# Kernel tuning notes

Measured on AMD Instinct MI355X. Metric: run time of the kernel, lower is better.

Reference implementation:

```python
import jax, jax.numpy as jnp
import numpy as np


def gcn_conv(x, W, b, src, dst, w, num_nodes):
    """PyG GCNConv: out = D^{-1/2} (A + I) D^{-1/2} (x @ W) + b, edge weights w."""
    xw = x @ W  # [BN, out_dim]
    # degree with self-loop weight 1.0, accumulated at target nodes
    deg = jax.ops.segment_sum(w, dst, num_segments=num_nodes) + 1.0  # [BN]
    dinv = jax.lax.rsqrt(deg)
    norm = dinv[src] * w * dinv[dst]  # [E]
    agg = jax.ops.segment_sum(xw[src] * norm[:, None], dst, num_segments=num_nodes)
    agg = agg + xw * (dinv * dinv)[:, None]  # self-loop contribution
    return agg + b


def setup_inputs() -> dict:
    key = jax.random.key(0)
    ks = jax.random.split(key, 10)
    BN, E, D = 100000, 1600000, 128
    return {
        "x": jax.random.normal(ks[0], (BN, D), dtype=jnp.float32),
        "edge_index": jax.random.randint(ks[1], (2, E), 0, BN, dtype=jnp.int64),
        "B": 8,
        "N": 12500,
        "causal_edge_index": jax.random.randint(ks[2], (2, 16), 0, BN, dtype=jnp.int64),
        "edge_weight": jax.random.uniform(ks[3], (E,), dtype=jnp.float32),
        "causal_edge_weight": jax.random.uniform(ks[4], (16,), dtype=jnp.float32),
        "W1": jax.random.normal(ks[5], (D, D), dtype=jnp.float32) * (1.0 / np.sqrt(D)),
        "b1": jnp.zeros((D,), dtype=jnp.float32),
        "W2": jax.random.normal(ks[6], (D, D), dtype=jnp.float32) * (1.0 / np.sqrt(D)),
        "b2": jnp.zeros((D,), dtype=jnp.float32),
        "Wres": jax.random.normal(ks[7], (D, D), dtype=jnp.float32) * (1.0 / np.sqrt(D)),
        "bres": jnp.zeros((D,), dtype=jnp.float32),
    }


def reference(x, edge_index, B, N, causal_edge_index, edge_weight,
              causal_edge_weight, W1, b1, W2, b2, Wres, bres):
    BN = B * N
    src, dst = edge_index[0], edge_index[1]
    # layer 1: GCNConv -> gelu (dropout is identity in eval)
    h = gcn_conv(x, W1, b1, src, dst, edge_weight, BN)  # [BN, hidden]
    h = jax.nn.gelu(h, approximate=False)
    # residual: 0.3 * Linear(x)
    h = h + 0.3 * (x @ Wres + bres)
    # layer 2: GCNConv -> gelu
    out = gcn_conv(h, W2, b2, src, dst, edge_weight, BN)
    return jax.nn.gelu(out, approximate=False)
```

## Files before the change

### kernel.cpp

```cpp
#include <hip/hip_runtime.h>
#include <math.h>

#define DIM 128
#define SCAN_CHUNK 4096
#define NB_HALF 256

typedef __attribute__((ext_vector_type(8))) short short8;
typedef __attribute__((ext_vector_type(4))) float f32x4;

__device__ __forceinline__ float gelu_exact(float v) {
    return 0.5f * v * (1.0f + erff(v * 0.70710678118654752f));
}

__device__ __forceinline__ unsigned short f2bf(float f) {
    unsigned int u = __float_as_uint(f);
    return (unsigned short)((u + 0x7FFFu + ((u >> 16) & 1u)) >> 16);
}
__device__ __forceinline__ float bf_lo(unsigned int v) { return __uint_as_float(v << 16); }
__device__ __forceinline__ float bf_hi(unsigned int v) { return __uint_as_float(v & 0xFFFF0000u); }


__global__ void deg_cnt_kernel(const int* __restrict__ dst,
                               const float* __restrict__ w,
                               unsigned long long* __restrict__ packed,
                               int* __restrict__ rank, int E) {
    int e = blockIdx.x * blockDim.x + threadIdx.x;
    if (e >= E) return;
    int d = dst[e];
    unsigned long long inc =
        (1ull << 32) | (unsigned long long)(unsigned int)(w[e] * 67108864.0f);
    unsigned long long old = atomicAdd(&packed[d], inc);
    rank[e] = (int)(old >> 32);
}


__global__ __launch_bounds__(256) void wt3_kernel(const float* __restrict__ W1,
                                                  const float* __restrict__ Wres,
                                                  const float* __restrict__ W2,
                                                  unsigned short* __restrict__ Wt1,
                                                  unsigned short* __restrict__ Wtr,
                                                  unsigned short* __restrict__ Wt2) {
    int b = blockIdx.x;
    const float* W = (b < 64) ? W1 : (b < 128) ? Wres : W2;
    unsigned short* Wt = (b < 64) ? Wt1 : (b < 128) ? Wtr : Wt2;
    int idx = (b & 63) * 256 + threadIdx.x;
    int r = idx >> 7, c = idx & 127;
    Wt[c * 128 + r] = f2bf(W[idx]);
}


template <int MODE>
__device__ __forceinline__ void gemm_breg_body(const float* __restrict__ X,
                                               const unsigned short* __restrict__ Wt,
                                               const float* __restrict__ bias,
                                               unsigned short* __restrict__ outb,
                                               float* __restrict__ Bf,
                                               int BN, int t0, int tStride) {
    int tid = threadIdx.x;
    int wv = tid >> 6, l = tid & 63;
    int l15 = l & 15, kg = l >> 4;

    uint4 b[4][8];
#pragma unroll
    for (int ks = 0; ks < 4; ks++)
#pragma unroll
        for (int nt = 0; nt < 8; nt++)
            b[ks][nt] = *(const uint4*)(Wt + (size_t)(nt * 16 + l15) * 128 + ks * 32 + kg * 8);

    float bias_r[8];
    if (MODE == 2) {
#pragma unroll
        for (int nt = 0; nt < 8; nt++) bias_r[nt] = bias[nt * 16 + l15];
    }

    int nTiles = (BN + 63) / 64;

    float4 aRaw[8];
    {
        int rowA = t0 * 64 + wv * 16 + l15;
        if (rowA > BN - 1) rowA = BN - 1;
        const float* ap = X + (size_t)rowA * 128 + kg * 8;
#pragma unroll
        for (int ks = 0; ks < 4; ks++) {
            aRaw[2 * ks] = *(const float4*)(ap + ks * 32);
            aRaw[2 * ks + 1] = *(const float4*)(ap + ks * 32 + 4);
        }
    }

    for (int t = t0; t < nTiles; t += tStride) {
        short8 aF[4];
#pragma unroll
        for (int ks = 0; ks < 4; ks++) {
            float4 a0 = aRaw[2 * ks], a1 = aRaw[2 * ks + 1];
            aF[ks][0] = (short)f2bf(a0.x); aF[ks][1] = (short)f2bf(a0.y);
            aF[ks][2] = (short)f2bf(a0.z); aF[ks][3] = (short)f2bf(a0.w);
            aF[ks][4] = (short)f2bf(a1.x); aF[ks][5] = (short)f2bf(a1.y);
            aF[ks][6] = (short)f2bf(a1.z); aF[ks][7] = (short)f2bf(a1.w);
        }
        int tn = t + tStride;
        if (tn < nTiles) {
            int rowA = tn * 64 + wv * 16 + l15;
            if (rowA > BN - 1) rowA = BN - 1;
            const float* ap = X + (size_t)rowA * 128 + kg * 8;
#pragma unroll
            for (int ks = 0; ks < 4; ks++) {
                aRaw[2 * ks] = *(const float4*)(ap + ks * 32);
                aRaw[2 * ks + 1] = *(const float4*)(ap + ks * 32 + 4);
            }
        }

        f32x4 acc[8];
#pragma unroll
        for (int nt = 0; nt < 8; nt++) acc[nt] = (f32x4){0.f, 0.f, 0.f, 0.f};
#pragma unroll
        for (int ks = 0; ks < 4; ks++)
#pragma unroll
            for (int nt = 0; nt < 8; nt++)
                acc[nt] = __builtin_amdgcn_mfma_f32_16x16x32_bf16(
                    aF[ks], __builtin_bit_cast(short8, b[ks][nt]), acc[nt], 0, 0, 0);

        int row0 = t * 64 + wv * 16;
#pragma unroll
        for (int nt = 0; nt < 8; nt++) {
            int col = nt * 16 + l15;
#pragma unroll
            for (int r = 0; r < 4; r++) {
                int row = row0 + kg * 4 + r;
                if (row >= BN) continue;
                size_t idx = (size_t)row * 128 + col;
                if (MODE == 0) outb[idx] = f2bf(acc[nt][r]);
                else           Bf[idx] = 0.3f * (acc[nt][r] + bias_r[nt]);
            }
        }
    }
}

__global__ __launch_bounds__(256, 2) void gemm2x_kernel(const float* __restrict__ x,
                                                        const unsigned short* __restrict__ Wt1,
                                                        const unsigned short* __restrict__ Wtr,
                                                        const float* __restrict__ bres,
                                                        unsigned short* __restrict__ Ab,
                                                        float* __restrict__ Bf, int BN) {
    int b = blockIdx.x;
    if (b < NB_HALF) gemm_breg_body<0>(x, Wt1, nullptr, Ab, nullptr, BN, b, NB_HALF);
    else             gemm_breg_body<2>(x, Wtr, bres, nullptr, Bf, BN, b - NB_HALF, NB_HALF);
}

__global__ __launch_bounds__(256, 2) void gemm1x_kernel(const float* __restrict__ X,
                                                        const unsigned short* __restrict__ Wt,
                                                        unsigned short* __restrict__ outb,
                                                        int BN) {
    gemm_breg_body<0>(X, Wt, nullptr, outb, nullptr, BN, blockIdx.x, 2 * NB_HALF);
}


__global__ __launch_bounds__(256) void scanAD_kernel(const unsigned long long* __restrict__ packed,
                                                     float* __restrict__ dinvf,
                                                     int* __restrict__ cnt,
                                                     int* __restrict__ partials, int BN) {
    int tid = threadIdx.x;
    int base = blockIdx.x * SCAN_CHUNK;
    int sum = 0;
#pragma unroll
    for (int i = 0; i < 16; i++) {
        int ii = base + i * 256 + tid;
        if (ii < BN) {
            unsigned long long v = packed[ii];
            int c = (int)(v >> 32);
            cnt[ii] = c;
            dinvf[ii] = rsqrtf((float)(unsigned int)(v & 0xFFFFFFFFu) * (1.0f / 67108864.0f) + 1.0f);
            sum += c;
        }
    }
    __shared__ int lds[4];
#pragma unroll
    for (int off = 32; off; off >>= 1) sum += __shfl_down(sum, off, 64);
    if ((tid & 63) == 0) lds[tid >> 6] = sum;
    __syncthreads();
    if (tid == 0) partials[blockIdx.x] = lds[0] + lds[1] + lds[2] + lds[3];
}

__global__ __launch_bounds__(256) void scanB_kernel(int* __restrict__ partials, int nblk) {
    __shared__ int lds[256];
    int tid = threadIdx.x;
    int v = (tid < nblk) ? partials[tid] : 0;
    lds[tid] = v;
    __syncthreads();
#pragma unroll
    for (int off = 1; off < 256; off <<= 1) {
        int t = (tid >= off) ? lds[tid - off] : 0;
        __syncthreads();
        lds[tid] += t;
        __syncthreads();
    }
    if (tid < nblk) partials[tid] = lds[tid] - v;
}

__global__ __launch_bounds__(256) void scanC_kernel(const int* __restrict__ cnt,
                                                    const int* __restrict__ partials,
                                                    int* __restrict__ ptr, int BN) {
    __shared__ int lds[256];
    int tid = threadIdx.x;
    int base = blockIdx.x * SCAN_CHUNK;
    int idx0 = base + tid * 16;
    int v[16];
    int tsum = 0;
#pragma unroll
    for (int j = 0; j < 16; j++) {
        int ii = idx0 + j;
        v[j] = (ii < BN) ? cnt[ii] : 0;
        tsum += v[j];
    }
    lds[tid] = tsum;
    __syncthreads();
#pragma unroll
    for (int off = 1; off < 256; off <<= 1) {
        int t = (tid >= off) ? lds[tid - off] : 0;
        __syncthreads();
        lds[tid] += t;
        __syncthreads();
    }
    int excl = lds[tid] - tsum + partials[blockIdx.x];
#pragma unroll
    for (int j = 0; j < 16; j++) {
        int ii = idx0 + j;
        if (ii < BN) ptr[ii] = excl;
        excl += v[j];
    }
}

__global__ void fill_kernel(const int* __restrict__ ei, const float* __restrict__ w,
                            const int* __restrict__ rank, const int* __restrict__ ptr,
                            const float* __restrict__ dinvf,
                            int2* __restrict__ csr, int E) {
    int e = blockIdx.x * blockDim.x + threadIdx.x;
    if (e >= E) return;
    int s = ei[e];
    int d = ei[(size_t)E + e];
    int pos = ptr[d] + rank[e];
    float nrm = dinvf[s] * w[e] * dinvf[d];
    csr[pos] = make_int2(s, __float_as_int(nrm));
}


template <int ACCMODE>
__global__ __launch_bounds__(256) void agg_kernel(const unsigned short* __restrict__ XWb,
                                                  const float* __restrict__ dinvf,
                                                  const int* __restrict__ ptr,
                                                  const int* __restrict__ cnt,
                                                  const int2* __restrict__ csr,
                                                  const float* __restrict__ bias,
                                                  float* __restrict__ out, int BN) {
    int h = threadIdx.x >> 5;
    int lane = threadIdx.x & 31;
    int n = blockIdx.x * 8 + h;
    if (n >= BN) return;
    int beg = ptr[n];
    int endv = beg + cnt[n];

    float4 a0 = make_float4(0.f, 0.f, 0.f, 0.f);
    float4 a1 = make_float4(0.f, 0.f, 0.f, 0.f);
    float4 a2 = make_float4(0.f, 0.f, 0.f, 0.f);
    float4 a3 = make_float4(0.f, 0.f, 0.f, 0.f);
    int i = beg;
    for (; i + 3 < endv; i += 4) {
        int2 e0 = csr[i], e1 = csr[i + 1], e2 = csr[i + 2], e3 = csr[i + 3];
        uint2 r0 = *(const uint2*)(XWb + (size_t)e0.x * 128 + lane * 4);
        uint2 r1 = *(const uint2*)(XWb + (size_t)e1.x * 128 + lane * 4);
        uint2 r2 = *(const uint2*)(XWb + (size_t)e2.x * 128 + lane * 4);
        uint2 r3 = *(const uint2*)(XWb + (size_t)e3.x * 128 + lane * 4);
        float n0 = __int_as_float(e0.y), n1 = __int_as_float(e1.y);
        float n2 = __int_as_float(e2.y), n3 = __int_as_float(e3.y);
        a0.x += n0 * bf_lo(r0.x); a0.y += n0 * bf_hi(r0.x);
        a0.z += n0 * bf_lo(r0.y); a0.w += n0 * bf_hi(r0.y);
        a1.x += n1 * bf_lo(r1.x); a1.y += n1 * bf_hi(r1.x);
        a1.z += n1 * bf_lo(r1.y); a1.w += n1 * bf_hi(r1.y);
        a2.x += n2 * bf_lo(r2.x); a2.y += n2 * bf_hi(r2.x);
        a2.z += n2 * bf_lo(r2.y); a2.w += n2 * bf_hi(r2.y);
        a3.x += n3 * bf_lo(r3.x); a3.y += n3 * bf_hi(r3.x);
        a3.z += n3 * bf_lo(r3.y); a3.w += n3 * bf_hi(r3.y);
    }
    for (; i < endv; i++) {
        int2 e0 = csr[i];
        uint2 r0 = *(const uint2*)(XWb + (size_t)e0.x * 128 + lane * 4);
        float n0 = __int_as_float(e0.y);
        a0.x += n0 * bf_lo(r0.x); a0.y += n0 * bf_hi(r0.x);
        a0.z += n0 * bf_lo(r0.y); a0.w += n0 * bf_hi(r0.y);
    }
    float dn = dinvf[n];
    float sl = dn * dn;
    uint2 rs = *(const uint2*)(XWb + (size_t)n * 128 + lane * 4);
    float4 bb = ((const float4*)bias)[lane];
    float4 o;
    o.x = gelu_exact(a0.x + a1.x + a2.x + a3.x + sl * bf_lo(rs.x) + bb.x);
    o.y = gelu_exact(a0.y + a1.y + a2.y + a3.y + sl * bf_hi(rs.x) + bb.y);
    o.z = gelu_exact(a0.z + a1.z + a2.z + a3.z + sl * bf_lo(rs.y) + bb.z);
    o.w = gelu_exact(a0.w + a1.w + a2.w + a3.w + sl * bf_hi(rs.y) + bb.w);
    float4* op = (float4*)(out + (size_t)n * 128) + lane;
    if (ACCMODE == 1) {
        float4 prev = *op;
        o.x += prev.x; o.y += prev.y; o.z += prev.z; o.w += prev.w;
    }
    *op = o;
}


extern "C" void kernel_launch(void* const* d_in, const int* in_sizes, int n_in,
                              void* d_out, int out_size, void* d_ws, size_t ws_size,
                              hipStream_t stream) {
    const float* x = (const float*)d_in[0];
    const int* ei = (const int*)d_in[1];
    const float* w = (const float*)d_in[5];
    const float* W1 = (const float*)d_in[7];
    const float* b1 = (const float*)d_in[8];
    const float* W2 = (const float*)d_in[9];
    const float* b2 = (const float*)d_in[10];
    const float* Wres = (const float*)d_in[11];
    const float* bres = (const float*)d_in[12];

    const int BN = in_sizes[0] / DIM;
    const int E = in_sizes[1] / 2;
    const int NBLK = (BN + SCAN_CHUNK - 1) / SCAN_CHUNK;

    char* p = (char*)d_ws;
    unsigned short* Ab = (unsigned short*)p;         p += (size_t)BN * DIM * 2;
    unsigned long long* packed = (unsigned long long*)p;  p += (size_t)BN * 8;
    float* dinvf = (float*)p;          p += (size_t)BN * 4;
    int* cnt = (int*)p;                p += (size_t)BN * 4;
    int* ptr = (int*)p;                p += (size_t)BN * 4;
    int* partials = (int*)p;           p += 1024;
    unsigned short* Wt1 = (unsigned short*)p;   p += 128 * 128 * 2;
    unsigned short* Wtr = (unsigned short*)p;   p += 128 * 128 * 2;
    unsigned short* Wt2 = (unsigned short*)p;   p += 128 * 128 * 2;
    int* rank = (int*)p;               p += (size_t)E * 4;
    int2* csr = (int2*)p;              p += (size_t)E * 8;

    float* Bf = (float*)d_out;

    const int* dst32 = ei + E;

    hipMemsetAsync(packed, 0, (size_t)BN * 8, stream);

    int tE = (E + 255) / 256;
    int aggBlocks = (BN + 7) / 8;

    deg_cnt_kernel<<<tE, 256, 0, stream>>>(dst32, w, packed, rank, E);
    wt3_kernel<<<192, 256, 0, stream>>>(W1, Wres, W2, Wt1, Wtr, Wt2);

    gemm2x_kernel<<<2 * NB_HALF, 256, 0, stream>>>(x, Wt1, Wtr, bres, Ab, Bf, BN);

    scanAD_kernel<<<NBLK, 256, 0, stream>>>(packed, dinvf, cnt, partials, BN);
    scanB_kernel<<<1, 256, 0, stream>>>(partials, NBLK);
    scanC_kernel<<<NBLK, 256, 0, stream>>>(cnt, partials, ptr, BN);
    fill_kernel<<<tE, 256, 0, stream>>>(ei, w, rank, ptr, dinvf, csr, E);

    agg_kernel<1><<<aggBlocks, 256, 0, stream>>>(Ab, dinvf, ptr, cnt, csr, b1, Bf, BN);

    gemm1x_kernel<<<2 * NB_HALF, 256, 0, stream>>>(Bf, Wt2, Ab, BN);
    agg_kernel<0><<<aggBlocks, 256, 0, stream>>>(Ab, dinvf, ptr, cnt, csr, b2, (float*)d_out, BN);
}
```

Before: 450.7 us.

## Replicate degree counters to spread atomic contention and factor dst normalization

The degree/count atomics now go to four replicated counter arrays chosen by edge index, so fewer same-address atomics collide. The scan merges the replicas and emits a per-replica sub-offset array used by the CSR fill. The fill also drops the dinv[dst] factor from each edge weight and the aggregation applies it once per node. This adds a larger memset, more scan reads and wider offset arrays, in exchange for less atomic serialization and one fewer gather per edge in the fill.

Result: no change. 458.3 us (+1.7%).

```diff
diff --git a/kernel.cpp b/kernel.cpp
--- a/kernel.cpp
+++ b/kernel.cpp
@@ -4,6 +4,7 @@
 #define DIM 128
 #define SCAN_CHUNK 4096
 #define NB_HALF 256
+#define NREP 4
 
 typedef __attribute__((ext_vector_type(8))) short short8;
 typedef __attribute__((ext_vector_type(4))) float f32x4;
@@ -22,14 +23,15 @@
 
 __global__ void deg_cnt_kernel(const int* __restrict__ dst,
                                const float* __restrict__ w,
-                               unsigned long long* __restrict__ packed,
-                               int* __restrict__ rank, int E) {
+                               unsigned long long* __restrict__ packedK,
+                               int* __restrict__ rank, int E, int BN) {
     int e = blockIdx.x * blockDim.x + threadIdx.x;
     if (e >= E) return;
     int d = dst[e];
+    int k = e & (NREP - 1);
     unsigned long long inc =
         (1ull << 32) | (unsigned long long)(unsigned int)(w[e] * 67108864.0f);
-    unsigned long long old = atomicAdd(&packed[d], inc);
+    unsigned long long old = atomicAdd(&packedK[(size_t)k * BN + d], inc);
     rank[e] = (int)(old >> 32);
 }
 
@@ -154,9 +156,10 @@
 }
 
 
-__global__ __launch_bounds__(256) void scanAD_kernel(const unsigned long long* __restrict__ packed,
+__global__ __launch_bounds__(256) void scanAD_kernel(const unsigned long long* __restrict__ packedK,
                                                      float* __restrict__ dinvf,
                                                      int* __restrict__ cnt,
+                                                     int4* __restrict__ offs,
                                                      int* __restrict__ partials, int BN) {
     int tid = threadIdx.x;
     int base = blockIdx.x * SCAN_CHUNK;
@@ -165,11 +168,19 @@
     for (int i = 0; i < 16; i++) {
         int ii = base + i * 256 + tid;
         if (ii < BN) {
-            unsigned long long v = packed[ii];
-            int c = (int)(v >> 32);
-            cnt[ii] = c;
-            dinvf[ii] = rsqrtf((float)(unsigned int)(v & 0xFFFFFFFFu) * (1.0f / 67108864.0f) + 1.0f);
-            sum += c;
+            int c[NREP];
+            unsigned int wlo = 0;
+#pragma unroll
+            for (int k = 0; k < NREP; k++) {
+                unsigned long long v = packedK[(size_t)k * BN + ii];
+                c[k] = (int)(v >> 32);
+                wlo += (unsigned int)(v & 0xFFFFFFFFu);
+            }
+            int ctot = c[0] + c[1] + c[2] + c[3];
+            cnt[ii] = ctot;
+            offs[ii] = make_int4(0, c[0], c[0] + c[1], c[0] + c[1] + c[2]);
+            dinvf[ii] = rsqrtf((float)wlo * (1.0f / 67108864.0f) + 1.0f);
+            sum += ctot;
         }
     }
     __shared__ int lds[4];
@@ -197,8 +208,9 @@
 }
 
 __global__ __launch_bounds__(256) void scanC_kernel(const int* __restrict__ cnt,
+                                                    const int4* __restrict__ offs,
                                                     const int* __restrict__ partials,
-                                                    int* __restrict__ ptr, int BN) {
+                                                    int4* __restrict__ po4, int BN) {
     __shared__ int lds[256];
     int tid = threadIdx.x;
     int base = blockIdx.x * SCAN_CHUNK;
@@ -224,29 +236,33 @@
 #pragma unroll
     for (int j = 0; j < 16; j++) {
         int ii = idx0 + j;
-        if (ii < BN) ptr[ii] = excl;
+        if (ii < BN) {
+            int4 o = offs[ii];
+            po4[ii] = make_int4(excl + o.x, excl + o.y, excl + o.z, excl + o.w);
+        }
         excl += v[j];
     }
 }
 
 __global__ void fill_kernel(const int* __restrict__ ei, const float* __restrict__ w,
-                            const int* __restrict__ rank, const int* __restrict__ ptr,
+                            const int* __restrict__ rank, const int* __restrict__ po4,
                             const float* __restrict__ dinvf,
                             int2* __restrict__ csr, int E) {
     int e = blockIdx.x * blockDim.x + threadIdx.x;
     if (e >= E) return;
     int s = ei[e];
     int d = ei[(size_t)E + e];
-    int pos = ptr[d] + rank[e];
-    float nrm = dinvf[s] * w[e] * dinvf[d];
-    csr[pos] = make_int2(s, __float_as_int(nrm));
+    int k = e & (NREP - 1);
+    int pos = po4[4 * d + k] + rank[e];
+    float v = dinvf[s] * w[e];
+    csr[pos] = make_int2(s, __float_as_int(v));
 }
 
 
 template <int ACCMODE>
 __global__ __launch_bounds__(256) void agg_kernel(const unsigned short* __restrict__ XWb,
                                                   const float* __restrict__ dinvf,
-                                                  const int* __restrict__ ptr,
+                                                  const int* __restrict__ ptr4,
                                                   const int* __restrict__ cnt,
                                                   const int2* __restrict__ csr,
                                                   const float* __restrict__ bias,
@@ -255,7 +271,7 @@
     int lane = threadIdx.x & 31;
     int n = blockIdx.x * 8 + h;
     if (n >= BN) return;
-    int beg = ptr[n];
+    int beg = ptr4[4 * n];
     int endv = beg + cnt[n];
 
     float4 a0 = make_float4(0.f, 0.f, 0.f, 0.f);
@@ -288,14 +304,13 @@
         a0.z += n0 * bf_lo(r0.y); a0.w += n0 * bf_hi(r0.y);
     }
     float dn = dinvf[n];
-    float sl = dn * dn;
     uint2 rs = *(const uint2*)(XWb + (size_t)n * 128 + lane * 4);
     float4 bb = ((const float4*)bias)[lane];
     float4 o;
-    o.x = gelu_exact(a0.x + a1.x + a2.x + a3.x + sl * bf_lo(rs.x) + bb.x);
-    o.y = gelu_exact(a0.y + a1.y + a2.y + a3.y + sl * bf_hi(rs.x) + bb.y);
-    o.z = gelu_exact(a0.z + a1.z + a2.z + a3.z + sl * bf_lo(rs.y) + bb.z);
-    o.w = gelu_exact(a0.w + a1.w + a2.w + a3.w + sl * bf_hi(rs.y) + bb.w);
+    o.x = gelu_exact(dn * (a0.x + a1.x + a2.x + a3.x + dn * bf_lo(rs.x)) + bb.x);
+    o.y = gelu_exact(dn * (a0.y + a1.y + a2.y + a3.y + dn * bf_hi(rs.x)) + bb.y);
+    o.z = gelu_exact(dn * (a0.z + a1.z + a2.z + a3.z + dn * bf_lo(rs.y)) + bb.z);
+    o.w = gelu_exact(dn * (a0.w + a1.w + a2.w + a3.w + dn * bf_hi(rs.y)) + bb.w);
     float4* op = (float4*)(out + (size_t)n * 128) + lane;
     if (ACCMODE == 1) {
         float4 prev = *op;
@@ -324,10 +339,11 @@
 
     char* p = (char*)d_ws;
     unsigned short* Ab = (unsigned short*)p;         p += (size_t)BN * DIM * 2;
-    unsigned long long* packed = (unsigned long long*)p;  p += (size_t)BN * 8;
+    unsigned long long* packedK = (unsigned long long*)p;  p += (size_t)NREP * BN * 8;
     float* dinvf = (float*)p;          p += (size_t)BN * 4;
     int* cnt = (int*)p;                p += (size_t)BN * 4;
-    int* ptr = (int*)p;                p += (size_t)BN * 4;
+    int4* offs = (int4*)p;             p += (size_t)BN * 16;
+    int4* po4 = (int4*)p;              p += (size_t)BN * 16;
     int* partials = (int*)p;           p += 1024;
     unsigned short* Wt1 = (unsigned short*)p;   p += 128 * 128 * 2;
     unsigned short* Wtr = (unsigned short*)p;   p += 128 * 128 * 2;
@@ -339,23 +355,23 @@
 
     const int* dst32 = ei + E;
 
-    hipMemsetAsync(packed, 0, (size_t)BN * 8, stream);
+    hipMemsetAsync(packedK, 0, (size_t)NREP * BN * 8, stream);
 
     int tE = (E + 255) / 256;
     int aggBlocks = (BN + 7) / 8;
 
-    deg_cnt_kernel<<<tE, 256, 0, stream>>>(dst32, w, packed, rank, E);
+    deg_cnt_kernel<<<tE, 256, 0, stream>>>(dst32, w, packedK, rank, E, BN);
     wt3_kernel<<<192, 256, 0, stream>>>(W1, Wres, W2, Wt1, Wtr, Wt2);
 
     gemm2x_kernel<<<2 * NB_HALF, 256, 0, stream>>>(x, Wt1, Wtr, bres, Ab, Bf, BN);
 
-    scanAD_kernel<<<NBLK, 256, 0, stream>>>(packed, dinvf, cnt, partials, BN);
+    scanAD_kernel<<<NBLK, 256, 0, stream>>>(packedK, dinvf, cnt, offs, partials, BN);
     scanB_kernel<<<1, 256, 0, stream>>>(partials, NBLK);
-    scanC_kernel<<<NBLK, 256, 0, stream>>>(cnt, partials, ptr, BN);
-    fill_kernel<<<tE, 256, 0, stream>>>(ei, w, rank, ptr, dinvf, csr, E);
-
-    agg_kernel<1><<<aggBlocks, 256, 0, stream>>>(Ab, dinvf, ptr, cnt, csr, b1, Bf, BN);
+    scanC_kernel<<<NBLK, 256, 0, stream>>>(cnt, offs, partials, po4, BN);
+    fill_kernel<<<tE, 256, 0, stream>>>(ei, w, rank, (const int*)po4, dinvf, csr, E);
+
+    agg_kernel<1><<<aggBlocks, 256, 0, stream>>>(Ab, dinvf, (const int*)po4, cnt, csr, b1, Bf, BN);
 
     gemm1x_kernel<<<2 * NB_HALF, 256, 0, stream>>>(Bf, Wt2, Ab, BN);
-    agg_kernel<0><<<aggBlocks, 256, 0, stream>>>(Ab, dinvf, ptr, cnt, csr, b2, (float*)d_out, BN);
-}
+    agg_kernel<0><<<aggBlocks, 256, 0, stream>>>(Ab, dinvf, (const int*)po4, cnt, csr, b2, (float*)d_out, BN);
+}
```
